# Kernel optimization log

Hardware: AMD Instinct MI355X
Metric: run time of the kernel (lower is better)

## Reference

```python
import jax, jax.numpy as jnp
import numpy as np

NUM_HEADS = 8
TAU = 2.0
BN_EPS = 1e-5


def _make_atan_spike(alpha):
    @jax.custom_vjp
    def spike(x):
        return (x >= 0.0).astype(x.dtype)
    def fwd(x):
        return spike(x), x
    def bwd(x, g):
        sg = (alpha / 2.0) / (1.0 + (jnp.pi / 2.0 * alpha * x) ** 2)
        return (g * sg,)
    spike.defvjp(fwd, bwd)
    return spike


def _make_sigmoid_spike(alpha):
    @jax.custom_vjp
    def spike(x):
        return (x >= 0.0).astype(x.dtype)
    def fwd(x):
        return spike(x), x
    def bwd(x, g):
        s = jax.nn.sigmoid(alpha * x)
        return (g * alpha * s * (1.0 - s),)
    spike.defvjp(fwd, bwd)
    return spike

_atan_spike = _make_atan_spike(5.0)       # surrogate.ATan(alpha=5.0)
_sigmoid_spike = _make_sigmoid_spike(4.0)  # spikingjelly default surrogate.Sigmoid(alpha=4.0)


def lif_multistep(x_seq, v_threshold, spike_fn):
    """Multi-step LIF, tau=2, hard reset to 0, detach_reset=True, decay_input=True.
    x_seq: [T, ...]. Returns spike sequence [T, ...]."""
    def step(v, x):
        h = v + (x - v) / TAU
        s = spike_fn(h - v_threshold)
        sd = jax.lax.stop_gradient(s)  # detach_reset
        v_new = h * (1.0 - sd)         # hard reset to v_reset=0
        return v_new, s
    _, s_seq = jax.lax.scan(step, jnp.zeros_like(x_seq[0]), x_seq)
    return s_seq


def bn(x, gamma, beta, mean, var):
    # inference-mode BatchNorm1d over channel dim C of [T,B,C,N]
    inv = gamma / jnp.sqrt(var + BN_EPS)
    return (x - mean[None, None, :, None]) * inv[None, None, :, None] + beta[None, None, :, None]


def setup_inputs() -> dict:
    key = jax.random.key(0)
    T, B, C, H, W = 4, 32, 384, 16, 16
    ks = jax.random.split(key, 20)
    d = {"x": jax.random.normal(ks[0], (T, B, C, H, W), dtype=jnp.float32)}
    std = 1.0 / np.sqrt(C)
    for i, p in enumerate(["q", "k", "proj"]):
        d[p + "_w"] = jax.random.normal(ks[1 + 5 * i], (C, C), dtype=jnp.float32) * std
        d[p + "_gamma"] = jnp.ones((C,), jnp.float32) + 0.1 * jax.random.normal(ks[2 + 5 * i], (C,))
        d[p + "_beta"] = 0.1 * jax.random.normal(ks[3 + 5 * i], (C,))
        d[p + "_mean"] = 0.1 * jax.random.normal(ks[4 + 5 * i], (C,))
        d[p + "_var"] = jax.random.uniform(ks[5 + 5 * i], (C,), minval=0.5, maxval=1.5)
    d["proj_b"] = 0.01 * jax.random.normal(ks[16], (C,))
    return d


def reference(x, q_w, q_gamma, q_beta, q_mean, q_var,
              k_w, k_gamma, k_beta, k_mean, k_var,
              proj_w, proj_gamma, proj_beta, proj_mean, proj_var, proj_b):
    T, B, C, H, W = x.shape
    N = H * W
    Ch = C // NUM_HEADS
    xf = x.reshape(T, B, C, N)

    # q branch: 1x1 conv (C x C matmul) -> BN -> LIF
    q = bn(jnp.einsum('tbcn,dc->tbdn', xf, q_w), q_gamma, q_beta, q_mean, q_var)
    q = lif_multistep(q, 1.0, _atan_spike)
    q = q.reshape(T, B, NUM_HEADS, Ch, N)
    q = jnp.sum(q, axis=3, keepdims=True)          # [T,B,h,1,N]
    attn = lif_multistep(q, 0.5, _sigmoid_spike)    # attn_lif, v_threshold=0.5

    # k branch
    k = bn(jnp.einsum('tbcn,dc->tbdn', xf, k_w), k_gamma, k_beta, k_mean, k_var)
    k = lif_multistep(k, 1.0, _atan_spike)
    k = k.reshape(T, B, NUM_HEADS, Ch, N)

    y = (attn * k).reshape(T, B, C, N)

    # proj: 1x1 conv with bias -> BN -> LIF
    y = jnp.einsum('tbcn,dc->tbdn', y, proj_w) + proj_b[None, None, :, None]
    y = bn(y, proj_gamma, proj_beta, proj_mean, proj_var)
    y = lif_multistep(y, 1.0, _atan_spike)
    return y.reshape(T, B, C, H, W)
```

## Files before the change

kernel.cpp:

```cpp
#include <hip/hip_runtime.h>

typedef _Float16 f16x8 __attribute__((ext_vector_type(8)));
typedef _Float16 f16x4 __attribute__((ext_vector_type(4)));
typedef float    f32x4 __attribute__((ext_vector_type(4)));

#define TT 4
#define BB 32
#define CC 384
#define NN 256

#define WS_X1   25165824
#define WS_WSP  50331648
#define WS_Y    52101120
#define WS_NEED 77266944

__global__ __launch_bounds__(256) void prep(
    const float* __restrict__ x,
    const float* __restrict__ qw, const float* __restrict__ kw,
    const float* __restrict__ pw,
    _Float16* __restrict__ x0, _Float16* __restrict__ x1,
    _Float16* __restrict__ wsp)
{
    __shared__ float xs[64 * 65];
    const int tid = threadIdx.x;
    int bid = blockIdx.x;

    if (bid >= 3072) {
        int gid   = (bid - 3072) * 256 + tid;
        int which = gid / 18432;
        int sid   = gid % 18432;
        int frag  = sid >> 6;
        int lane  = sid & 63;
        int h  = frag / 36;
        int rm = frag % 36;
        int dt = rm / 12, kc = rm % 12;
        int m16 = lane & 15, quad = lane >> 4;
        int d = h * 48 + dt * 16 + m16;

        const float* src = (which == 0) ? qw : (which == 1) ? kw : pw;
        _Float16* o0 = wsp + (size_t)which * 294912;
        _Float16* o1 = o0 + 147456;

        f16x8 h0, h1;
#pragma unroll
        for (int jj = 0; jj < 8; ++jj) {
            int cp = kc * 32 + quad * 8 + jj;
            int c;
            if (which == 2) {
                int hp = cp / 48, w = cp % 48;
                int qp = w / 12, r12 = w % 12;
                int sl = r12 >> 2, rr = r12 & 3;
                c = hp * 48 + sl * 16 + qp * 4 + rr;
            } else {
                c = cp;
            }
            float v = src[d * CC + c];
            _Float16 a = (_Float16)v;
            h0[jj] = a; h1[jj] = (_Float16)(v - (float)a);
        }
        size_t off = (size_t)frag * 512 + lane * 8;
        *(f16x8*)(o0 + off) = h0;
        *(f16x8*)(o1 + off) = h1;
        return;
    }

    int tb = bid / 24, r = bid % 24;
    int c0 = (r >> 2) * 64, n0 = (r & 3) * 64;

#pragma unroll
    for (int p = 0; p < 4; ++p) {
        int c  = (tid >> 4) + p * 16;
        int nl = (tid & 15) * 4;
        float4 v = *(const float4*)&x[((size_t)tb * CC + c0 + c) * NN + n0 + nl];
        *(float4*)&xs[c * 65 + nl] = v;
    }
    __syncthreads();
#pragma unroll
    for (int p = 0; p < 2; ++p) {
        int sid  = p * 256 + tid;
        int frag = sid >> 6;
        int lane = sid & 63;
        int kcl  = frag & 1, n16l = frag >> 1;
        int m16 = lane & 15, quad = lane >> 4;
        int n_local = n16l * 16 + m16;
        int c_local = kcl * 32 + quad * 8;
        f16x8 h0, h1;
#pragma unroll
        for (int jj = 0; jj < 8; ++jj) {
            float v = xs[(c_local + jj) * 65 + n_local];
            _Float16 a = (_Float16)v;
            h0[jj] = a; h1[jj] = (_Float16)(v - (float)a);
        }
        size_t gf = ((size_t)tb * 16 + (n0 >> 4) + n16l) * 12 + (c0 >> 5) + kcl;
        size_t off = gf * 512 + lane * 8;
        *(f16x8*)(x0 + off) = h0;
        *(f16x8*)(x1 + off) = h1;
    }
}

#define QK_LOADX(dst, kcv)                                                   \
    {                                                                        \
        _Pragma("unroll")                                                    \
        for (int t = 0; t < 4; ++t) {                                        \
            dst[t][0] = *(const f16x8*)(pxb0[t] + (kcv) * 512 + lo);         \
            dst[t][1] = *(const f16x8*)(pxb1[t] + (kcv) * 512 + lo);         \
        }                                                                    \
    }

#define QK_STEP(kcv, bxv)                                                    \
    {                                                                        \
        f16x8 w[4][3];                                                       \
        _Pragma("unroll")                                                    \
        for (int brs = 0; brs < 4; ++brs)                                    \
            _Pragma("unroll")                                                \
            for (int dt = 0; dt < 3; ++dt)                                   \
                w[brs][dt] = *(const f16x8*)(wt[brs] +                       \
                    (dt * 12 + (kcv)) * 512 + lo);                           \
        _Pragma("unroll")                                                    \
        for (int dt = 0; dt < 3; ++dt) {                                     \
            _Pragma("unroll")                                                \
            for (int t = 0; t < 4; ++t) {                                    \
                f32x4 cq = aq[t][dt];                                        \
                cq = __builtin_amdgcn_mfma_f32_16x16x32_f16(w[0][dt], bxv[t][0], cq, 0, 0, 0); \
                cq = __builtin_amdgcn_mfma_f32_16x16x32_f16(w[1][dt], bxv[t][0], cq, 0, 0, 0); \
                cq = __builtin_amdgcn_mfma_f32_16x16x32_f16(w[0][dt], bxv[t][1], cq, 0, 0, 0); \
                aq[t][dt] = cq;                                              \
                f32x4 ck = ak[t][dt];                                        \
                ck = __builtin_amdgcn_mfma_f32_16x16x32_f16(w[2][dt], bxv[t][0], ck, 0, 0, 0); \
                ck = __builtin_amdgcn_mfma_f32_16x16x32_f16(w[3][dt], bxv[t][0], ck, 0, 0, 0); \
                ck = __builtin_amdgcn_mfma_f32_16x16x32_f16(w[2][dt], bxv[t][1], ck, 0, 0, 0); \
                ak[t][dt] = ck;                                              \
            }                                                                \
        }                                                                    \
    }

__global__ __launch_bounds__(256, 2) void qk_mfma(
    const _Float16* __restrict__ x0, const _Float16* __restrict__ x1,
    const _Float16* __restrict__ wsp,
    const float* __restrict__ qg, const float* __restrict__ qbe,
    const float* __restrict__ qm, const float* __restrict__ qva,
    const float* __restrict__ kg, const float* __restrict__ kbe,
    const float* __restrict__ km, const float* __restrict__ kva,
    _Float16* __restrict__ y)
{
    const int tid  = threadIdx.x;
    const int wave = tid >> 6;
    const int lane = tid & 63;
    const int m16  = lane & 15;
    const int quad = lane >> 4;
    const int lo   = lane * 8;

    int bid = blockIdx.x;
    int r   = bid & 7;
    int hh  = (bid >> 3) & 1;
    int qq  = bid >> 4;
    int j   = qq * 8 + r;
    int b   = j >> 4;
    int n16 = j & 15;

    const int head = hh * 4 + wave;

    const _Float16* pxb0[4];
    const _Float16* pxb1[4];
#pragma unroll
    for (int t = 0; t < 4; ++t) {
        size_t off = (((size_t)(t * BB + b) * 16 + n16) * 12) * 512;
        pxb0[t] = x0 + off;
        pxb1[t] = x1 + off;
    }
    const _Float16* wt[4];
#pragma unroll
    for (int brs = 0; brs < 4; ++brs)
        wt[brs] = wsp + (size_t)brs * 147456 + (size_t)head * 36 * 512;

    f32x4 aq[4][3], ak[4][3];
#pragma unroll
    for (int t = 0; t < 4; ++t)
#pragma unroll
        for (int dt = 0; dt < 3; ++dt) {
            aq[t][dt] = (f32x4){0.f, 0.f, 0.f, 0.f};
            ak[t][dt] = (f32x4){0.f, 0.f, 0.f, 0.f};
        }

    f16x8 bxA[4][2], bxB[4][2];
    QK_LOADX(bxA, 0)
#pragma unroll
    for (int kc2 = 0; kc2 < 6; ++kc2) {
        QK_LOADX(bxB, 2 * kc2 + 1)
        QK_STEP(2 * kc2, bxA)
        if (kc2 < 5)
            QK_LOADX(bxA, 2 * kc2 + 2)
        QK_STEP(2 * kc2 + 1, bxB)
    }

    float invq[3][4], invk[3][4];
    f32x4 mqv[3], bqv[3], mkv[3], bkv[3];
#pragma unroll
    for (int dt = 0; dt < 3; ++dt) {
        int doff = head * 48 + dt * 16 + quad * 4;
        f32x4 gq  = *(const f32x4*)(qg + doff);
        f32x4 vq_ = *(const f32x4*)(qva + doff);
        f32x4 gk_ = *(const f32x4*)(kg + doff);
        f32x4 vk_ = *(const f32x4*)(kva + doff);
        mqv[dt] = *(const f32x4*)(qm + doff);
        bqv[dt] = *(const f32x4*)(qbe + doff);
        mkv[dt] = *(const f32x4*)(km + doff);
        bkv[dt] = *(const f32x4*)(kbe + doff);
#pragma unroll
        for (int rr = 0; rr < 4; ++rr) {
            invq[dt][rr] = gq[rr] / sqrtf(vq_[rr] + 1e-5f);
            invk[dt][rr] = gk_[rr] / sqrtf(vk_[rr] + 1e-5f);
        }
    }

    f32x4 vq[3], vk[3];
    float va = 0.f;
#pragma unroll
    for (int dt = 0; dt < 3; ++dt) {
        vq[dt] = (f32x4){0.f, 0.f, 0.f, 0.f};
        vk[dt] = (f32x4){0.f, 0.f, 0.f, 0.f};
    }
#pragma unroll
    for (int t = 0; t < 4; ++t) {
        float psum = 0.f;
        f32x4 ks[3];
#pragma unroll
        for (int dt = 0; dt < 3; ++dt) {
#pragma unroll
            for (int rr = 0; rr < 4; ++rr) {
                float bnq = (aq[t][dt][rr] - mqv[dt][rr]) * invq[dt][rr] + bqv[dt][rr];
                float hq  = vq[dt][rr] + (bnq - vq[dt][rr]) * 0.5f;
                float sq  = (hq - 1.0f >= 0.0f) ? 1.0f : 0.0f;
                vq[dt][rr] = hq * (1.0f - sq);
                psum += sq;
                float bnk = (ak[t][dt][rr] - mkv[dt][rr]) * invk[dt][rr] + bkv[dt][rr];
                float hk  = vk[dt][rr] + (bnk - vk[dt][rr]) * 0.5f;
                float sk  = (hk - 1.0f >= 0.0f) ? 1.0f : 0.0f;
                vk[dt][rr] = hk * (1.0f - sk);
                ks[dt][rr] = sk;
            }
        }
        psum += __shfl_xor(psum, 16, 64);
        psum += __shfl_xor(psum, 32, 64);
        float ha = va + (psum - va) * 0.5f;
        float sa = (ha - 0.5f >= 0.0f) ? 1.0f : 0.0f;
        va = ha * (1.0f - sa);
        float attn = sa;
        size_t ybase = (((size_t)(t * BB + b) * 16 + n16) * 12) * 512;
#pragma unroll
        for (int dt = 0; dt < 3; ++dt) {
            int c   = head * 48 + quad * 12 + dt * 4;
            int kcy = c >> 5;
            int qp  = (c & 31) >> 3;
            int jj  = c & 7;
            f16x4 hv;
#pragma unroll
            for (int rr = 0; rr < 4; ++rr)
                hv[rr] = (_Float16)(attn * ks[dt][rr]);
            *(f16x4*)(y + ybase + (size_t)kcy * 512 + (m16 + 16 * qp) * 8 + jj) = hv;
        }
    }
}

#define PJ_LOADY(dst, kcv)                                                   \
    {                                                                        \
        _Pragma("unroll")                                                    \
        for (int t = 0; t < 4; ++t)                                          \
            dst[t] = *(const f16x8*)(pyb[t] + (kcv) * 512 + lo);             \
    }

#define PJ_STEP(kcv, byv)                                                    \
    {                                                                        \
        f16x8 w[2][3];                                                       \
        _Pragma("unroll")                                                    \
        for (int sp = 0; sp < 2; ++sp)                                       \
            _Pragma("unroll")                                                \
            for (int dt = 0; dt < 3; ++dt)                                   \
                w[sp][dt] = *(const f16x8*)(pwt[sp] +                        \
                    (dt * 12 + (kcv)) * 512 + lo);                           \
        _Pragma("unroll")                                                    \
        for (int dt = 0; dt < 3; ++dt) {                                     \
            _Pragma("unroll")                                                \
            for (int t = 0; t < 4; ++t) {                                    \
                f32x4 c = acc[t][dt];                                        \
                c = __builtin_amdgcn_mfma_f32_16x16x32_f16(w[0][dt], byv[t], c, 0, 0, 0); \
                c = __builtin_amdgcn_mfma_f32_16x16x32_f16(w[1][dt], byv[t], c, 0, 0, 0); \
                acc[t][dt] = c;                                              \
            }                                                                \
        }                                                                    \
    }

__global__ __launch_bounds__(256, 2) void proj_mfma(
    const _Float16* __restrict__ y,
    const _Float16* __restrict__ pw0, const _Float16* __restrict__ pw1,
    const float* __restrict__ pg, const float* __restrict__ pbe,
    const float* __restrict__ pm, const float* __restrict__ pva,
    const float* __restrict__ pbias, float* __restrict__ out)
{
    const int tid  = threadIdx.x;
    const int wave = tid >> 6;
    const int lane = tid & 63;
    const int m16  = lane & 15;
    const int quad = lane >> 4;
    const int lo   = lane * 8;

    int bid = blockIdx.x;
    int r   = bid & 7;
    int dgg = (bid >> 3) & 1;
    int qq  = bid >> 4;
    int j   = qq * 8 + r;
    int b   = j >> 4;
    int n16 = j & 15;

    const int dw = dgg * 4 + wave;
    const int d0 = dw * 48;

    const _Float16* pyb[4];
#pragma unroll
    for (int t = 0; t < 4; ++t)
        pyb[t] = y + (((size_t)(t * BB + b) * 16 + n16) * 12) * 512;
    const _Float16* pwt[2];
    pwt[0] = pw0 + (size_t)dw * 36 * 512;
    pwt[1] = pw1 + (size_t)dw * 36 * 512;

    f32x4 acc[4][3];
#pragma unroll
    for (int t = 0; t < 4; ++t)
#pragma unroll
        for (int dt = 0; dt < 3; ++dt)
            acc[t][dt] = (f32x4){0.f, 0.f, 0.f, 0.f};

    f16x8 byA[4], byB[4];
    PJ_LOADY(byA, 0)
#pragma unroll
    for (int kc2 = 0; kc2 < 6; ++kc2) {
        PJ_LOADY(byB, 2 * kc2 + 1)
        PJ_STEP(2 * kc2, byA)
        if (kc2 < 5)
            PJ_LOADY(byA, 2 * kc2 + 2)
        PJ_STEP(2 * kc2 + 1, byB)
    }

    f32x4 vv[3];
#pragma unroll
    for (int dt = 0; dt < 3; ++dt) vv[dt] = (f32x4){0.f, 0.f, 0.f, 0.f};
#pragma unroll
    for (int dt = 0; dt < 3; ++dt) {
        int doff = d0 + dt * 16 + quad * 4;
        f32x4 g_  = *(const f32x4*)(pg + doff);
        f32x4 be  = *(const f32x4*)(pbe + doff);
        f32x4 mu  = *(const f32x4*)(pm + doff);
        f32x4 va_ = *(const f32x4*)(pva + doff);
        f32x4 bi  = *(const f32x4*)(pbias + doff);
        float inv[4];
#pragma unroll
        for (int rr = 0; rr < 4; ++rr)
            inv[rr] = g_[rr] / sqrtf(va_[rr] + 1e-5f);
#pragma unroll
        for (int t = 0; t < 4; ++t) {
#pragma unroll
            for (int rr = 0; rr < 4; ++rr) {
                float z  = acc[t][dt][rr] + bi[rr];
                float bn = (z - mu[rr]) * inv[rr] + be[rr];
                float h  = vv[dt][rr] + (bn - vv[dt][rr]) * 0.5f;
                float sp = (h - 1.0f >= 0.0f) ? 1.0f : 0.0f;
                vv[dt][rr] = h * (1.0f - sp);
                out[((size_t)(t * BB + b) * CC + doff + rr) * NN +
                    n16 * 16 + m16] = sp;
            }
        }
    }
}

#define KC 64
#define LSTR 68
__global__ __launch_bounds__(256) void qk_fused(
    const float* __restrict__ x,
    const float* __restrict__ qw, const float* __restrict__ qg,
    const float* __restrict__ qbe, const float* __restrict__ qm,
    const float* __restrict__ qva,
    const float* __restrict__ kw, const float* __restrict__ kg,
    const float* __restrict__ kbe, const float* __restrict__ km,
    const float* __restrict__ kva,
    unsigned char* __restrict__ y)
{
    __shared__ float xs[KC * LSTR];
    __shared__ float qws[48 * LSTR];
    __shared__ float kws[48 * LSTR];
    __shared__ float hsum[16 * 64];
    const int tid = threadIdx.x, bid = blockIdx.x;
    const int b = bid >> 5, head = (bid >> 2) & 7, n0 = (bid & 3) << 6;
    const int dg = tid >> 4, nl = (tid & 15) << 2;
    float q_inv[3], q_mu[3], q_b[3], k_inv[3], k_mu[3], k_b[3];
#pragma unroll
    for (int i = 0; i < 3; ++i) {
        int d = head * 48 + dg * 3 + i;
        q_inv[i] = qg[d] / sqrtf(qva[d] + 1e-5f); q_mu[i] = qm[d]; q_b[i] = qbe[d];
        k_inv[i] = kg[d] / sqrtf(kva[d] + 1e-5f); k_mu[i] = km[d]; k_b[i] = kbe[d];
    }
    float vq[3][4] = {}, vk[3][4] = {}, va[4] = {};
    for (int t = 0; t < TT; ++t) {
        float accq[3][4] = {}, acck[3][4] = {};
        for (int kc = 0; kc < CC / KC; ++kc) {
            const int c0 = kc * KC;
            __syncthreads();
#pragma unroll
            for (int p = 0; p < 4; ++p) {
                int q4 = tid + p * 256, cc = q4 >> 4, nn = (q4 & 15) << 2;
                *(float4*)&xs[cc * LSTR + nn] =
                    *(const float4*)&x[((size_t)(t * BB + b) * CC + c0 + cc) * NN + n0 + nn];
            }
#pragma unroll
            for (int p = 0; p < 3; ++p) {
                int q4 = tid + p * 256, dl = q4 >> 4, cc = (q4 & 15) << 2;
                *(float4*)&qws[dl * LSTR + cc] = *(const float4*)&qw[(head * 48 + dl) * CC + c0 + cc];
                *(float4*)&kws[dl * LSTR + cc] = *(const float4*)&kw[(head * 48 + dl) * CC + c0 + cc];
            }
            __syncthreads();
#pragma unroll
            for (int cq = 0; cq < KC / 4; ++cq) {
                float xv[4][4];
#pragma unroll
                for (int uu = 0; uu < 4; ++uu)
                    *(float4*)&xv[uu][0] = *(const float4*)&xs[(cq * 4 + uu) * LSTR + nl];
#pragma unroll
                for (int i = 0; i < 3; ++i) {
                    float qv[4], kv[4];
                    *(float4*)&qv[0] = *(const float4*)&qws[(dg * 3 + i) * LSTR + cq * 4];
                    *(float4*)&kv[0] = *(const float4*)&kws[(dg * 3 + i) * LSTR + cq * 4];
#pragma unroll
                    for (int uu = 0; uu < 4; ++uu)
#pragma unroll
                        for (int jj = 0; jj < 4; ++jj) {
                            accq[i][jj] = fmaf(qv[uu], xv[uu][jj], accq[i][jj]);
                            acck[i][jj] = fmaf(kv[uu], xv[uu][jj], acck[i][jj]);
                        }
                }
            }
        }
        float part[4] = {0.f, 0.f, 0.f, 0.f};
        float ksp[3][4];
#pragma unroll
        for (int i = 0; i < 3; ++i)
#pragma unroll
            for (int jj = 0; jj < 4; ++jj) {
                float bnq = (accq[i][jj] - q_mu[i]) * q_inv[i] + q_b[i];
                float hq = vq[i][jj] + (bnq - vq[i][jj]) * 0.5f;
                float sq = (hq - 1.0f >= 0.0f) ? 1.0f : 0.0f;
                vq[i][jj] = hq * (1.0f - sq); part[jj] += sq;
                float bnk = (acck[i][jj] - k_mu[i]) * k_inv[i] + k_b[i];
                float hk = vk[i][jj] + (bnk - vk[i][jj]) * 0.5f;
                float sk = (hk - 1.0f >= 0.0f) ? 1.0f : 0.0f;
                vk[i][jj] = hk * (1.0f - sk); ksp[i][jj] = sk;
            }
#pragma unroll
        for (int jj = 0; jj < 4; ++jj) hsum[dg * 64 + nl + jj] = part[jj];
        __syncthreads();
        float attn[4];
#pragma unroll
        for (int jj = 0; jj < 4; ++jj) {
            float tot = 0.f;
#pragma unroll
            for (int g = 0; g < 16; ++g) tot += hsum[g * 64 + nl + jj];
            float ha = va[jj] + (tot - va[jj]) * 0.5f;
            float sa = (ha - 0.5f >= 0.0f) ? 1.0f : 0.0f;
            va[jj] = ha * (1.0f - sa); attn[jj] = sa;
        }
#pragma unroll
        for (int i = 0; i < 3; ++i) {
            uchar4 yo;
            yo.x = (unsigned char)(attn[0] * ksp[i][0]);
            yo.y = (unsigned char)(attn[1] * ksp[i][1]);
            yo.z = (unsigned char)(attn[2] * ksp[i][2]);
            yo.w = (unsigned char)(attn[3] * ksp[i][3]);
            *(uchar4*)&((unsigned char*)y)[((size_t)(t * BB + b) * CC + head * 48 + dg * 3 + i) * NN + n0 + nl] = yo;
        }
    }
}

__global__ __launch_bounds__(256) void proj_fused(
    const unsigned char* __restrict__ yin,
    const float* __restrict__ pw, const float* __restrict__ pg,
    const float* __restrict__ pbe, const float* __restrict__ pm,
    const float* __restrict__ pva, const float* __restrict__ pbias,
    float* __restrict__ out)
{
    __shared__ float ys[KC * LSTR];
    __shared__ float pws[64 * LSTR];
    const int tid = threadIdx.x, bid = blockIdx.x;
    const int b = bid / 24, r = bid % 24, d0 = (r >> 2) * 64, n0 = (r & 3) << 6;
    const int dg = tid >> 4, nl = (tid & 15) << 2;
    float inv[4], mu[4], be[4], bi[4];
#pragma unroll
    for (int i = 0; i < 4; ++i) {
        int d = d0 + dg * 4 + i;
        inv[i] = pg[d] / sqrtf(pva[d] + 1e-5f);
        mu[i] = pm[d]; be[i] = pbe[d]; bi[i] = pbias[d];
    }
    float vvv[4][4] = {};
    for (int t = 0; t < TT; ++t) {
        float acc[4][4] = {};
        for (int kc = 0; kc < CC / KC; ++kc) {
            const int c0 = kc * KC;
            __syncthreads();
#pragma unroll
            for (int p = 0; p < 4; ++p) {
                int q4 = tid + p * 256, cc = q4 >> 4, nn = (q4 & 15) << 2;
                unsigned int w = *(const unsigned int*)&yin[((size_t)(t * BB + b) * CC + c0 + cc) * NN + n0 + nn];
                ys[cc * LSTR + nn + 0] = (float)(w & 0xff);
                ys[cc * LSTR + nn + 1] = (float)((w >> 8) & 0xff);
                ys[cc * LSTR + nn + 2] = (float)((w >> 16) & 0xff);
                ys[cc * LSTR + nn + 3] = (float)(w >> 24);
                *(float4*)&pws[cc * LSTR + nn] = *(const float4*)&pw[(d0 + cc) * CC + c0 + nn];
            }
            __syncthreads();
#pragma unroll
            for (int cq = 0; cq < KC / 4; ++cq) {
                float xv[4][4];
#pragma unroll
                for (int uu = 0; uu < 4; ++uu)
                    *(float4*)&xv[uu][0] = *(const float4*)&ys[(cq * 4 + uu) * LSTR + nl];
#pragma unroll
                for (int i = 0; i < 4; ++i) {
                    float pv[4];
                    *(float4*)&pv[0] = *(const float4*)&pws[(dg * 4 + i) * LSTR + cq * 4];
#pragma unroll
                    for (int uu = 0; uu < 4; ++uu)
#pragma unroll
                        for (int jj = 0; jj < 4; ++jj)
                            acc[i][jj] = fmaf(pv[uu], xv[uu][jj], acc[i][jj]);
                }
            }
        }
#pragma unroll
        for (int i = 0; i < 4; ++i) {
            float res[4];
#pragma unroll
            for (int jj = 0; jj < 4; ++jj) {
                float z = acc[i][jj] + bi[i];
                float bnv = (z - mu[i]) * inv[i] + be[i];
                float h = vvv[i][jj] + (bnv - vvv[i][jj]) * 0.5f;
                float sx = (h - 1.0f >= 0.0f) ? 1.0f : 0.0f;
                vvv[i][jj] = h * (1.0f - sx);
                res[jj] = sx;
            }
            *(float4*)&out[((size_t)(t * BB + b) * CC + d0 + dg * 4 + i) * NN + n0 + nl] = *(float4*)&res[0];
        }
    }
}

extern "C" void kernel_launch(void* const* d_in, const int* in_sizes, int n_in,
                              void* d_out, int out_size, void* d_ws, size_t ws_size,
                              hipStream_t stream)
{
    const float* x     = (const float*)d_in[0];
    const float* qw    = (const float*)d_in[1];
    const float* qg    = (const float*)d_in[2];
    const float* qbe   = (const float*)d_in[3];
    const float* qm    = (const float*)d_in[4];
    const float* qva   = (const float*)d_in[5];
    const float* kw    = (const float*)d_in[6];
    const float* kg    = (const float*)d_in[7];
    const float* kbe   = (const float*)d_in[8];
    const float* km    = (const float*)d_in[9];
    const float* kva   = (const float*)d_in[10];
    const float* pw    = (const float*)d_in[11];
    const float* pg    = (const float*)d_in[12];
    const float* pbe   = (const float*)d_in[13];
    const float* pm    = (const float*)d_in[14];
    const float* pva   = (const float*)d_in[15];
    const float* pbias = (const float*)d_in[16];
    float* out = (float*)d_out;

    if (ws_size >= (size_t)WS_NEED) {
        char* w = (char*)d_ws;
        _Float16* x0  = (_Float16*)(w);
        _Float16* x1  = (_Float16*)(w + WS_X1);
        _Float16* wsp = (_Float16*)(w + WS_WSP);
        _Float16* pw0 = wsp + 4 * 147456;
        _Float16* pw1 = wsp + 5 * 147456;
        _Float16* yf  = (_Float16*)(w + WS_Y);

        prep<<<3288, 256, 0, stream>>>(x, qw, kw, pw, x0, x1, wsp);
        qk_mfma<<<1024, 256, 0, stream>>>(x0, x1, wsp, qg, qbe, qm, qva,
                                          kg, kbe, km, kva, yf);
        proj_mfma<<<1024, 256, 0, stream>>>(yf, pw0, pw1, pg, pbe, pm, pva,
                                            pbias, out);
    } else {
        unsigned char* y = (unsigned char*)d_ws;
        qk_fused<<<BB * 8 * (NN / 64), 256, 0, stream>>>(
            x, qw, qg, qbe, qm, qva, kw, kg, kbe, km, kva, y);
        proj_fused<<<BB * (CC / 64) * (NN / 64), 256, 0, stream>>>(
            y, pw, pg, pbe, pm, pva, pbias, out);
    }
}
```

Measured before the change: 222.2 us.

## Split QK time steps into two halves to cut registers, raise occupancy

The QK kernel now processes the four time steps in two passes of two, so only half the accumulators and x fragments are live at once. BN parameters are reloaded and recomputed inside the epilogue instead of being kept live across the GEMM. Both QK and proj kernels request three blocks per CU via launch bounds. The aim is lower register pressure and higher occupancy, at the cost of loading weights twice per block and repeating the BN division and sqrt.

```diff
diff --git a/kernel.cpp b/kernel.cpp
--- a/kernel.cpp
+++ b/kernel.cpp
@@ -98,43 +98,47 @@
     }
 }
 
-#define QK_LOADX(dst, kcv)                                                   \
-    {                                                                        \
-        _Pragma("unroll")                                                    \
-        for (int t = 0; t < 4; ++t) {                                        \
-            dst[t][0] = *(const f16x8*)(pxb0[t] + (kcv) * 512 + lo);         \
-            dst[t][1] = *(const f16x8*)(pxb1[t] + (kcv) * 512 + lo);         \
-        }                                                                    \
-    }
-
-#define QK_STEP(kcv, bxv)                                                    \
-    {                                                                        \
-        f16x8 w[4][3];                                                       \
-        _Pragma("unroll")                                                    \
-        for (int brs = 0; brs < 4; ++brs)                                    \
-            _Pragma("unroll")                                                \
-            for (int dt = 0; dt < 3; ++dt)                                   \
-                w[brs][dt] = *(const f16x8*)(wt[brs] +                       \
-                    (dt * 12 + (kcv)) * 512 + lo);                           \
-        _Pragma("unroll")                                                    \
-        for (int dt = 0; dt < 3; ++dt) {                                     \
-            _Pragma("unroll")                                                \
-            for (int t = 0; t < 4; ++t) {                                    \
-                f32x4 cq = aq[t][dt];                                        \
-                cq = __builtin_amdgcn_mfma_f32_16x16x32_f16(w[0][dt], bxv[t][0], cq, 0, 0, 0); \
-                cq = __builtin_amdgcn_mfma_f32_16x16x32_f16(w[1][dt], bxv[t][0], cq, 0, 0, 0); \
-                cq = __builtin_amdgcn_mfma_f32_16x16x32_f16(w[0][dt], bxv[t][1], cq, 0, 0, 0); \
-                aq[t][dt] = cq;                                              \
-                f32x4 ck = ak[t][dt];                                        \
-                ck = __builtin_amdgcn_mfma_f32_16x16x32_f16(w[2][dt], bxv[t][0], ck, 0, 0, 0); \
-                ck = __builtin_amdgcn_mfma_f32_16x16x32_f16(w[3][dt], bxv[t][0], ck, 0, 0, 0); \
-                ck = __builtin_amdgcn_mfma_f32_16x16x32_f16(w[2][dt], bxv[t][1], ck, 0, 0, 0); \
-                ak[t][dt] = ck;                                              \
-            }                                                                \
-        }                                                                    \
-    }
-
-__global__ __launch_bounds__(256, 2) void qk_mfma(
+__device__ __forceinline__ void qk_loadx2(
+    const _Float16* __restrict__ x0, const _Float16* __restrict__ x1,
+    const size_t* fx, int kc, f16x8 bx[2][2])
+{
+#pragma unroll
+    for (int t2 = 0; t2 < 2; ++t2) {
+        bx[t2][0] = *(const f16x8*)(x0 + fx[t2] + kc * 512);
+        bx[t2][1] = *(const f16x8*)(x1 + fx[t2] + kc * 512);
+    }
+}
+
+__device__ __forceinline__ void qk_step2(
+    const _Float16* __restrict__ wq0, const _Float16* __restrict__ wq1,
+    const _Float16* __restrict__ wk0, const _Float16* __restrict__ wk1,
+    size_t fwb, int kc, const f16x8 bx[2][2],
+    f32x4 aq[2][3], f32x4 ak[2][3])
+{
+#pragma unroll
+    for (int dt = 0; dt < 3; ++dt) {
+        size_t wo = fwb + (size_t)(dt * 12 + kc) * 512;
+        f16x8 q0 = *(const f16x8*)(wq0 + wo);
+        f16x8 q1 = *(const f16x8*)(wq1 + wo);
+        f16x8 k0 = *(const f16x8*)(wk0 + wo);
+        f16x8 k1 = *(const f16x8*)(wk1 + wo);
+#pragma unroll
+        for (int t2 = 0; t2 < 2; ++t2) {
+            f32x4 cq = aq[t2][dt];
+            cq = __builtin_amdgcn_mfma_f32_16x16x32_f16(q0, bx[t2][0], cq, 0, 0, 0);
+            cq = __builtin_amdgcn_mfma_f32_16x16x32_f16(q1, bx[t2][0], cq, 0, 0, 0);
+            cq = __builtin_amdgcn_mfma_f32_16x16x32_f16(q0, bx[t2][1], cq, 0, 0, 0);
+            aq[t2][dt] = cq;
+            f32x4 ck = ak[t2][dt];
+            ck = __builtin_amdgcn_mfma_f32_16x16x32_f16(k0, bx[t2][0], ck, 0, 0, 0);
+            ck = __builtin_amdgcn_mfma_f32_16x16x32_f16(k1, bx[t2][0], ck, 0, 0, 0);
+            ck = __builtin_amdgcn_mfma_f32_16x16x32_f16(k0, bx[t2][1], ck, 0, 0, 0);
+            ak[t2][dt] = ck;
+        }
+    }
+}
+
+__global__ __launch_bounds__(256, 3) void qk_mfma(
     const _Float16* __restrict__ x0, const _Float16* __restrict__ x1,
     const _Float16* __restrict__ wsp,
     const float* __restrict__ qg, const float* __restrict__ qbe,
@@ -148,7 +152,6 @@
     const int lane = tid & 63;
     const int m16  = lane & 15;
     const int quad = lane >> 4;
-    const int lo   = lane * 8;
 
     int bid = blockIdx.x;
     int r   = bid & 7;
@@ -160,58 +163,16 @@
 
     const int head = hh * 4 + wave;
 
-    const _Float16* pxb0[4];
-    const _Float16* pxb1[4];
-#pragma unroll
-    for (int t = 0; t < 4; ++t) {
-        size_t off = (((size_t)(t * BB + b) * 16 + n16) * 12) * 512;
-        pxb0[t] = x0 + off;
-        pxb1[t] = x1 + off;
-    }
-    const _Float16* wt[4];
-#pragma unroll
-    for (int brs = 0; brs < 4; ++brs)
-        wt[brs] = wsp + (size_t)brs * 147456 + (size_t)head * 36 * 512;
-
-    f32x4 aq[4][3], ak[4][3];
+    const _Float16* wq0 = wsp;
+    const _Float16* wq1 = wsp + 147456;
+    const _Float16* wk0 = wsp + 2 * 147456;
+    const _Float16* wk1 = wsp + 3 * 147456;
+
+    size_t fxb[4];
 #pragma unroll
     for (int t = 0; t < 4; ++t)
-#pragma unroll
-        for (int dt = 0; dt < 3; ++dt) {
-            aq[t][dt] = (f32x4){0.f, 0.f, 0.f, 0.f};
-            ak[t][dt] = (f32x4){0.f, 0.f, 0.f, 0.f};
-        }
-
-    f16x8 bxA[4][2], bxB[4][2];
-    QK_LOADX(bxA, 0)
-#pragma unroll
-    for (int kc2 = 0; kc2 < 6; ++kc2) {
-        QK_LOADX(bxB, 2 * kc2 + 1)
-        QK_STEP(2 * kc2, bxA)
-        if (kc2 < 5)
-            QK_LOADX(bxA, 2 * kc2 + 2)
-        QK_STEP(2 * kc2 + 1, bxB)
-    }
-
-    float invq[3][4], invk[3][4];
-    f32x4 mqv[3], bqv[3], mkv[3], bkv[3];
-#pragma unroll
-    for (int dt = 0; dt < 3; ++dt) {
-        int doff = head * 48 + dt * 16 + quad * 4;
-        f32x4 gq  = *(const f32x4*)(qg + doff);
-        f32x4 vq_ = *(const f32x4*)(qva + doff);
-        f32x4 gk_ = *(const f32x4*)(kg + doff);
-        f32x4 vk_ = *(const f32x4*)(kva + doff);
-        mqv[dt] = *(const f32x4*)(qm + doff);
-        bqv[dt] = *(const f32x4*)(qbe + doff);
-        mkv[dt] = *(const f32x4*)(km + doff);
-        bkv[dt] = *(const f32x4*)(kbe + doff);
-#pragma unroll
-        for (int rr = 0; rr < 4; ++rr) {
-            invq[dt][rr] = gq[rr] / sqrtf(vq_[rr] + 1e-5f);
-            invk[dt][rr] = gk_[rr] / sqrtf(vk_[rr] + 1e-5f);
-        }
-    }
+        fxb[t] = (((size_t)(t * BB + b) * 16 + n16) * 12) * 512 + lane * 8;
+    size_t fwb = ((size_t)head * 36) * 512 + lane * 8;
 
     f32x4 vq[3], vk[3];
     float va = 0.f;
@@ -220,44 +181,80 @@
         vq[dt] = (f32x4){0.f, 0.f, 0.f, 0.f};
         vk[dt] = (f32x4){0.f, 0.f, 0.f, 0.f};
     }
-#pragma unroll
-    for (int t = 0; t < 4; ++t) {
-        float psum = 0.f;
-        f32x4 ks[3];
-#pragma unroll
-        for (int dt = 0; dt < 3; ++dt) {
-#pragma unroll
-            for (int rr = 0; rr < 4; ++rr) {
-                float bnq = (aq[t][dt][rr] - mqv[dt][rr]) * invq[dt][rr] + bqv[dt][rr];
-                float hq  = vq[dt][rr] + (bnq - vq[dt][rr]) * 0.5f;
-                float sq  = (hq - 1.0f >= 0.0f) ? 1.0f : 0.0f;
-                vq[dt][rr] = hq * (1.0f - sq);
-                psum += sq;
-                float bnk = (ak[t][dt][rr] - mkv[dt][rr]) * invk[dt][rr] + bkv[dt][rr];
-                float hk  = vk[dt][rr] + (bnk - vk[dt][rr]) * 0.5f;
-                float sk  = (hk - 1.0f >= 0.0f) ? 1.0f : 0.0f;
-                vk[dt][rr] = hk * (1.0f - sk);
-                ks[dt][rr] = sk;
-            }
-        }
-        psum += __shfl_xor(psum, 16, 64);
-        psum += __shfl_xor(psum, 32, 64);
-        float ha = va + (psum - va) * 0.5f;
-        float sa = (ha - 0.5f >= 0.0f) ? 1.0f : 0.0f;
-        va = ha * (1.0f - sa);
-        float attn = sa;
-        size_t ybase = (((size_t)(t * BB + b) * 16 + n16) * 12) * 512;
-#pragma unroll
-        for (int dt = 0; dt < 3; ++dt) {
-            int c   = head * 48 + quad * 12 + dt * 4;
-            int kcy = c >> 5;
-            int qp  = (c & 31) >> 3;
-            int jj  = c & 7;
-            f16x4 hv;
-#pragma unroll
-            for (int rr = 0; rr < 4; ++rr)
-                hv[rr] = (_Float16)(attn * ks[dt][rr]);
-            *(f16x4*)(y + ybase + (size_t)kcy * 512 + (m16 + 16 * qp) * 8 + jj) = hv;
+
+    for (int tp = 0; tp < 2; ++tp) {
+        const size_t* fx = &fxb[tp * 2];
+        f32x4 aq[2][3], ak[2][3];
+#pragma unroll
+        for (int t2 = 0; t2 < 2; ++t2)
+#pragma unroll
+            for (int dt = 0; dt < 3; ++dt) {
+                aq[t2][dt] = (f32x4){0.f, 0.f, 0.f, 0.f};
+                ak[t2][dt] = (f32x4){0.f, 0.f, 0.f, 0.f};
+            }
+
+        f16x8 bxA[2][2], bxB[2][2];
+        qk_loadx2(x0, x1, fx, 0, bxA);
+#pragma unroll
+        for (int kc2 = 0; kc2 < 6; ++kc2) {
+            qk_loadx2(x0, x1, fx, 2 * kc2 + 1, bxB);
+            qk_step2(wq0, wq1, wk0, wk1, fwb, 2 * kc2, bxA, aq, ak);
+            if (kc2 < 5)
+                qk_loadx2(x0, x1, fx, 2 * kc2 + 2, bxA);
+            qk_step2(wq0, wq1, wk0, wk1, fwb, 2 * kc2 + 1, bxB, aq, ak);
+        }
+
+#pragma unroll
+        for (int t2 = 0; t2 < 2; ++t2) {
+            int t = tp * 2 + t2;
+            float psum = 0.f;
+            f32x4 ks[3];
+#pragma unroll
+            for (int dt = 0; dt < 3; ++dt) {
+                int doff = head * 48 + dt * 16 + quad * 4;
+                f32x4 gq  = *(const f32x4*)(qg + doff);
+                f32x4 bq  = *(const f32x4*)(qbe + doff);
+                f32x4 mq  = *(const f32x4*)(qm + doff);
+                f32x4 vq_ = *(const f32x4*)(qva + doff);
+                f32x4 gk_ = *(const f32x4*)(kg + doff);
+                f32x4 bk_ = *(const f32x4*)(kbe + doff);
+                f32x4 mk_ = *(const f32x4*)(km + doff);
+                f32x4 vk_ = *(const f32x4*)(kva + doff);
+#pragma unroll
+                for (int rr = 0; rr < 4; ++rr) {
+                    float invq = gq[rr] / sqrtf(vq_[rr] + 1e-5f);
+                    float invk = gk_[rr] / sqrtf(vk_[rr] + 1e-5f);
+                    float bnq = (aq[t2][dt][rr] - mq[rr]) * invq + bq[rr];
+                    float hq  = vq[dt][rr] + (bnq - vq[dt][rr]) * 0.5f;
+                    float sq  = (hq - 1.0f >= 0.0f) ? 1.0f : 0.0f;
+                    vq[dt][rr] = hq * (1.0f - sq);
+                    psum += sq;
+                    float bnk = (ak[t2][dt][rr] - mk_[rr]) * invk + bk_[rr];
+                    float hk  = vk[dt][rr] + (bnk - vk[dt][rr]) * 0.5f;
+                    float sk  = (hk - 1.0f >= 0.0f) ? 1.0f : 0.0f;
+                    vk[dt][rr] = hk * (1.0f - sk);
+                    ks[dt][rr] = sk;
+                }
+            }
+            psum += __shfl_xor(psum, 16, 64);
+            psum += __shfl_xor(psum, 32, 64);
+            float ha = va + (psum - va) * 0.5f;
+            float sa = (ha - 0.5f >= 0.0f) ? 1.0f : 0.0f;
+            va = ha * (1.0f - sa);
+            float attn = sa;
+            size_t ybase = (((size_t)(t * BB + b) * 16 + n16) * 12) * 512;
+#pragma unroll
+            for (int dt = 0; dt < 3; ++dt) {
+                int c   = head * 48 + quad * 12 + dt * 4;
+                int kcy = c >> 5;
+                int qp  = (c & 31) >> 3;
+                int jj  = c & 7;
+                f16x4 hv;
+#pragma unroll
+                for (int rr = 0; rr < 4; ++rr)
+                    hv[rr] = (_Float16)(attn * ks[dt][rr]);
+                *(f16x4*)(y + ybase + (size_t)kcy * 512 + (m16 + 16 * qp) * 8 + jj) = hv;
+            }
         }
     }
 }
@@ -290,7 +287,7 @@
         }                                                                    \
     }
 
-__global__ __launch_bounds__(256, 2) void proj_mfma(
+__global__ __launch_bounds__(256, 3) void proj_mfma(
     const _Float16* __restrict__ y,
     const _Float16* __restrict__ pw0, const _Float16* __restrict__ pw1,
     const float* __restrict__ pg, const float* __restrict__ pbe,
```

Measured after the change: 763.3 us. 243% more time.
